# Kernel tuning notes

Hardware: AMD Instinct MI355X
Metric: run time of the kernel (lower is better)

The kernel has to match this reference:

```python
import jax, jax.numpy as jnp
import numpy as np

N = 200000      # number of source simplices (columns of B)
M_SEG = 100000  # number of target simplices (rows of B)
NNZ = 400000    # ~2 nonzeros per column for a boundary operator
C_IN = 256
C_OUT = 256


def setup_inputs() -> dict:
    key = jax.random.key(0)
    k1, k2, k3, k4, k5 = jax.random.split(key, 5)
    x_src = jax.random.normal(k1, (N, C_IN), dtype=jnp.float32)
    W = jax.random.normal(k2, (C_IN, C_OUT), dtype=jnp.float32) / np.sqrt(C_IN)
    b_vals = jax.random.normal(k3, (NNZ,), dtype=jnp.float32)
    b_rows = jax.random.randint(k4, (NNZ,), 0, M_SEG, dtype=jnp.int32)
    b_cols = jax.random.randint(k5, (NNZ,), 0, N, dtype=jnp.int32)
    return {"x_src": x_src, "W": W, "b_vals": b_vals,
            "b_rows": b_rows, "b_cols": b_cols, "M": M_SEG}


def reference(x_src, W, b_vals, b_rows, b_cols, M):
    # Dense projection: nn.Linear(in, out, bias=False) -> x @ W
    x_proj = x_src @ W                                  # [N, C_out]
    # Sparse boundary matmul: out[r] += v * x_proj[c] for each (r, c, v) in B
    msgs = b_vals[:, None] * x_proj[b_cols]             # [nnz, C_out] gather
    out = jax.ops.segment_sum(msgs, b_rows, num_segments=M)  # [M, C_out] scatter-add
    return out
```

## Files before the change

### kernel.cpp

```cpp
#include <hip/hip_runtime.h>


typedef short bf16x8 __attribute__((ext_vector_type(8)));
typedef float f32x4  __attribute__((ext_vector_type(4)));

#define BM 64

static __device__ __forceinline__ unsigned short f2bf(float f) {
    union { float f; unsigned u; } a; a.f = f;
    unsigned r = a.u + 0x7FFFu + ((a.u >> 16) & 1u);
    return (unsigned short)(r >> 16);
}

__global__ __launch_bounds__(256) void wtrans_kernel(
    const float* __restrict__ W, unsigned short* __restrict__ Wt)
{
    int k = blockIdx.x;
    int n = threadIdx.x;
    Wt[(size_t)n * 256 + k] = f2bf(W[(size_t)k * 256 + n]);
}

__global__ __launch_bounds__(256) void hist_kernel(
    const int* __restrict__ b_rows, int* __restrict__ cnt, int nnz)
{
    int i = blockIdx.x * 256 + threadIdx.x;
    if (i < nnz) atomicAdd(&cnt[b_rows[i]], 1);
}

__global__ __launch_bounds__(1024) void scan_part_kernel(
    const int* __restrict__ cnt, int* __restrict__ partials, int M)
{
    int tid = threadIdx.x;
    int base = blockIdx.x * 4096;
    int s = 0;
    #pragma unroll
    for (int k = 0; k < 4; ++k) {
        int i = base + k * 1024 + tid;
        if (i < M) s += cnt[i];
    }
    #pragma unroll
    for (int d = 1; d < 64; d <<= 1) s += __shfl_xor(s, d);
    __shared__ int wsum[16];
    int lane = tid & 63, wid = tid >> 6;
    if (lane == 0) wsum[wid] = s;
    __syncthreads();
    if (tid == 0) {
        int t = 0;
        #pragma unroll
        for (int w = 0; w < 16; ++w) t += wsum[w];
        partials[blockIdx.x] = t;
    }
}

__global__ __launch_bounds__(64) void scan_mid_kernel(
    int* __restrict__ partials, int* __restrict__ off, int np, int M)
{
    int lane = threadIdx.x;
    int v = (lane < np) ? partials[lane] : 0;
    int x = v;
    #pragma unroll
    for (int d = 1; d < 64; d <<= 1) { int y = __shfl_up(x, d); if (lane >= d) x += y; }
    if (lane < np) partials[lane] = x - v;
    if (lane == 63) off[M] = x;
}

__global__ __launch_bounds__(1024) void scan_apply_kernel(
    const int* __restrict__ cnt, const int* __restrict__ partials,
    int* __restrict__ off, int* __restrict__ cursor, int M)
{
    int tid = threadIdx.x;
    int base = blockIdx.x * 4096 + tid * 4;
    int4 v = make_int4(0, 0, 0, 0);
    if (base + 3 < M) v = *reinterpret_cast<const int4*>(cnt + base);
    else {
        if (base + 0 < M) v.x = cnt[base + 0];
        if (base + 1 < M) v.y = cnt[base + 1];
        if (base + 2 < M) v.z = cnt[base + 2];
    }
    int s1 = v.x + v.y, s2 = s1 + v.z, tsum = s2 + v.w;
    int x = tsum;
    int lane = tid & 63, wid = tid >> 6;
    #pragma unroll
    for (int d = 1; d < 64; d <<= 1) { int y = __shfl_up(x, d); if (lane >= d) x += y; }
    __shared__ int wsum[16];
    if (lane == 63) wsum[wid] = x;
    __syncthreads();
    if (wid == 0 && lane < 16) {
        int w = wsum[lane];
        int xx = w;
        #pragma unroll
        for (int d = 1; d < 16; d <<= 1) { int y = __shfl_up(xx, d); if (lane >= d) xx += y; }
        wsum[lane] = xx - w;
    }
    __syncthreads();
    int excl = (x - tsum) + wsum[wid] + partials[blockIdx.x];
    int o0 = excl, o1 = excl + v.x, o2 = excl + s1, o3 = excl + s2;
    if (base + 0 < M) { off[base + 0] = o0; cursor[base + 0] = o0; }
    if (base + 1 < M) { off[base + 1] = o1; cursor[base + 1] = o1; }
    if (base + 2 < M) { off[base + 2] = o2; cursor[base + 2] = o2; }
    if (base + 3 < M) { off[base + 3] = o3; cursor[base + 3] = o3; }
}

__global__ __launch_bounds__(256) void fill_kernel(
    const float* __restrict__ b_vals, const int* __restrict__ b_rows,
    const int* __restrict__ b_cols, int* __restrict__ cursor,
    int* __restrict__ csr_col, float* __restrict__ csr_val, int nnz)
{
    int i = blockIdx.x * 256 + threadIdx.x;
    if (i < nnz) {
        int r = b_rows[i];
        int pos = atomicAdd(&cursor[r], 1);
        csr_col[pos] = b_cols[i];
        csr_val[pos] = b_vals[i];
    }
}

__global__ __launch_bounds__(256) void fused_kernel(
    const float* __restrict__ x_src, const float* __restrict__ csr_val,
    const int* __restrict__ csr_col, const int* __restrict__ off,
    const unsigned short* __restrict__ Wt, float* __restrict__ out, int M)
{
    __shared__ __align__(16) unsigned char Alds[BM * 512];

    int lane = threadIdx.x & 63;
    int wid  = threadIdx.x >> 6;
    int r0   = blockIdx.x * BM;

    const float4* x4 = reinterpret_cast<const float4*>(x_src);
    for (int i = 0; i < 16; ++i) {
        int row = wid * 16 + i;
        int r = r0 + row;
        float4 acc = make_float4(0.f, 0.f, 0.f, 0.f);
        if (r < M) {
            int s = off[r], e = off[r + 1];
            for (int j = s; j < e; ++j) {
                int c = csr_col[j];
                float v = csr_val[j];
                float4 xs = x4[(size_t)c * 64 + lane];
                acc.x += v * xs.x; acc.y += v * xs.y;
                acc.z += v * xs.z; acc.w += v * xs.w;
            }
        }
        ushort4 h;
        h.x = f2bf(acc.x); h.y = f2bf(acc.y); h.z = f2bf(acc.z); h.w = f2bf(acc.w);
        int byte = row * 512 + lane * 8;
        byte ^= (row & 7) << 4;
        *reinterpret_cast<ushort4*>(Alds + byte) = h;
    }
    __syncthreads();

    f32x4 acc[4][4] = {};
    const char* wt = reinterpret_cast<const char*>(Wt);
    int nbase = wid * 64;
    int arow15 = lane & 15;
    int kgrp   = (lane >> 4) * 16;

    for (int s = 0; s < 8; ++s) {
        bf16x8 a[4], b[4];
        #pragma unroll
        for (int m = 0; m < 4; ++m) {
            int row = m * 16 + arow15;
            int byte = row * 512 + s * 64 + kgrp;
            byte ^= (row & 7) << 4;
            a[m] = *reinterpret_cast<const bf16x8*>(Alds + byte);
        }
        #pragma unroll
        for (int t = 0; t < 4; ++t) {
            int n = nbase + t * 16 + arow15;
            b[t] = *reinterpret_cast<const bf16x8*>(wt + (size_t)n * 512 + s * 64 + kgrp);
        }
        #pragma unroll
        for (int m = 0; m < 4; ++m)
            #pragma unroll
            for (int t = 0; t < 4; ++t)
                acc[m][t] = __builtin_amdgcn_mfma_f32_16x16x32_bf16(a[m], b[t], acc[m][t], 0, 0, 0);
    }

    #pragma unroll
    for (int m = 0; m < 4; ++m) {
        int rowb = r0 + m * 16 + (lane >> 4) * 4;
        #pragma unroll
        for (int r = 0; r < 4; ++r) {
            if (rowb + r < M) {
                #pragma unroll
                for (int t = 0; t < 4; ++t)
                    out[(size_t)(rowb + r) * 256 + nbase + t * 16 + arow15] = acc[m][t][r];
            }
        }
    }
}

extern "C" void kernel_launch(void* const* d_in, const int* in_sizes, int n_in,
                              void* d_out, int out_size, void* d_ws, size_t ws_size,
                              hipStream_t stream) {
    const float* x_src  = (const float*)d_in[0];
    const float* W      = (const float*)d_in[1];
    const float* b_vals = (const float*)d_in[2];
    const int*   b_rows = (const int*)d_in[3];
    const int*   b_cols = (const int*)d_in[4];

    const int C = 256;
    const int M = out_size / C;
    const int nnz = in_sizes[2];

    char* ws = (char*)d_ws;
    unsigned short* Wt = (unsigned short*)ws;           ws += 256 * 256 * 2;
    int*   cnt     = (int*)ws;                          ws += (size_t)M * 4;
    int*   off     = (int*)ws;                          ws += (size_t)(M + 1) * 4;
    int*   cursor  = (int*)ws;                          ws += (size_t)M * 4;
    int*   partials= (int*)ws;                          ws += 64 * 4;
    int*   csr_col = (int*)ws;                          ws += (size_t)nnz * 4;
    float* csr_val = (float*)ws;                        ws += (size_t)nnz * 4;

    float* out = (float*)d_out;

    hipMemsetAsync(cnt, 0, (size_t)M * 4, stream);

    wtrans_kernel<<<256, 256, 0, stream>>>(W, Wt);

    int nblk_nnz = (nnz + 255) / 256;
    hist_kernel<<<nblk_nnz, 256, 0, stream>>>(b_rows, cnt, nnz);

    int nb = (M + 4095) / 4096;
    scan_part_kernel<<<nb, 1024, 0, stream>>>(cnt, partials, M);
    scan_mid_kernel<<<1, 64, 0, stream>>>(partials, off, nb, M);
    scan_apply_kernel<<<nb, 1024, 0, stream>>>(cnt, partials, off, cursor, M);

    fill_kernel<<<nblk_nnz, 256, 0, stream>>>(b_vals, b_rows, b_cols, cursor,
                                              csr_col, csr_val, nnz);

    int nblk_fused = (M + BM - 1) / BM;
    fused_kernel<<<nblk_fused, 256, 0, stream>>>(x_src, csr_val, csr_col, off,
                                                 Wt, out, M);
}
```

Baseline: 236.4 us.

## Balance sparse gather across waves with LDS atomics and packed row indices

The gather phase no longer assigns 16 fixed rows to each wave. Instead the block's whole nonzero range is split across waves two entries at a time, and each contribution is added into an fp32 LDS accumulator with atomics. The local row index is packed into the upper bits of the column word, and the row tile is halved to 32 to fit the larger LDS footprint. This targets load imbalance and serial per-row latency chains, at the cost of LDS atomic traffic, an extra pass converting to bf16, and a column range limited to 18 bits.

```diff
diff --git a/kernel.cpp b/kernel.cpp
--- a/kernel.cpp
+++ b/kernel.cpp
@@ -4,7 +4,7 @@
 typedef short bf16x8 __attribute__((ext_vector_type(8)));
 typedef float f32x4  __attribute__((ext_vector_type(4)));
 
-#define BM 64
+#define BM 32
 
 static __device__ __forceinline__ unsigned short f2bf(float f) {
     union { float f; unsigned u; } a; a.f = f;
@@ -104,87 +104,110 @@
 __global__ __launch_bounds__(256) void fill_kernel(
     const float* __restrict__ b_vals, const int* __restrict__ b_rows,
     const int* __restrict__ b_cols, int* __restrict__ cursor,
-    int* __restrict__ csr_col, float* __restrict__ csr_val, int nnz)
+    unsigned int* __restrict__ csr_packed, float* __restrict__ csr_val, int nnz)
 {
     int i = blockIdx.x * 256 + threadIdx.x;
     if (i < nnz) {
         int r = b_rows[i];
         int pos = atomicAdd(&cursor[r], 1);
-        csr_col[pos] = b_cols[i];
+        csr_packed[pos] = (unsigned)b_cols[i] | ((unsigned)(r & (BM - 1)) << 18);
         csr_val[pos] = b_vals[i];
     }
 }
 
 __global__ __launch_bounds__(256) void fused_kernel(
     const float* __restrict__ x_src, const float* __restrict__ csr_val,
-    const int* __restrict__ csr_col, const int* __restrict__ off,
+    const unsigned int* __restrict__ csr_packed, const int* __restrict__ off,
     const unsigned short* __restrict__ Wt, float* __restrict__ out, int M)
 {
-    __shared__ __align__(16) unsigned char Alds[BM * 512];
-
-    int lane = threadIdx.x & 63;
-    int wid  = threadIdx.x >> 6;
-    int r0   = blockIdx.x * BM;
-
-    const float4* x4 = reinterpret_cast<const float4*>(x_src);
-    for (int i = 0; i < 16; ++i) {
-        int row = wid * 16 + i;
-        int r = r0 + row;
-        float4 acc = make_float4(0.f, 0.f, 0.f, 0.f);
-        if (r < M) {
-            int s = off[r], e = off[r + 1];
-            for (int j = s; j < e; ++j) {
-                int c = csr_col[j];
-                float v = csr_val[j];
-                float4 xs = x4[(size_t)c * 64 + lane];
-                acc.x += v * xs.x; acc.y += v * xs.y;
-                acc.z += v * xs.z; acc.w += v * xs.w;
-            }
-        }
-        ushort4 h;
-        h.x = f2bf(acc.x); h.y = f2bf(acc.y); h.z = f2bf(acc.z); h.w = f2bf(acc.w);
-        int byte = row * 512 + lane * 8;
-        byte ^= (row & 7) << 4;
-        *reinterpret_cast<ushort4*>(Alds + byte) = h;
-    }
-    __syncthreads();
-
-    f32x4 acc[4][4] = {};
+    __shared__ __align__(16) float accf[BM * 256];
+    __shared__ __align__(16) unsigned char Ab[BM * 512];
+
+    int tid = threadIdx.x;
+    int lane = tid & 63, wid = tid >> 6;
+    int r0 = blockIdx.x * BM;
+
+    f32x4* az = reinterpret_cast<f32x4*>(accf);
+    #pragma unroll
+    for (int i = 0; i < (BM * 256 / 4) / 256; ++i)
+        az[i * 256 + tid] = (f32x4){0.f, 0.f, 0.f, 0.f};
+    __syncthreads();
+
+    int s_blk = off[r0];
+    int e_blk = off[min(r0 + BM, M)];
+
+    for (int j0 = s_blk + wid * 2; j0 < e_blk; j0 += 8) {
+        int j1 = j0 + 1;
+        bool has1 = (j1 < e_blk);
+        unsigned p0 = csr_packed[j0];
+        float    v0 = csr_val[j0];
+        unsigned p1 = has1 ? csr_packed[j1] : p0;
+        float    v1 = has1 ? csr_val[j1] : 0.f;
+        int c0 = (int)(p0 & 0x3FFFFu), a0 = (int)(p0 >> 18);
+        int c1 = (int)(p1 & 0x3FFFFu), a1 = (int)(p1 >> 18);
+
+        const float* s0 = x_src + (size_t)c0 * 256 + lane;
+        const float* s1 = x_src + (size_t)c1 * 256 + lane;
+        float g00 = s0[0], g01 = s0[64], g02 = s0[128], g03 = s0[192];
+        float g10 = s1[0], g11 = s1[64], g12 = s1[128], g13 = s1[192];
+
+        float* d0 = accf + a0 * 256 + lane;
+        float* d1 = accf + a1 * 256 + lane;
+        atomicAdd(d0 +   0, v0 * g00);
+        atomicAdd(d0 +  64, v0 * g01);
+        atomicAdd(d0 + 128, v0 * g02);
+        atomicAdd(d0 + 192, v0 * g03);
+        atomicAdd(d1 +   0, v1 * g10);
+        atomicAdd(d1 +  64, v1 * g11);
+        atomicAdd(d1 + 128, v1 * g12);
+        atomicAdd(d1 + 192, v1 * g13);
+    }
+    __syncthreads();
+
+    for (int e = tid * 2; e < BM * 256; e += 512) {
+        int row = e >> 8, ch = e & 255;
+        float2 f = *reinterpret_cast<const float2*>(accf + row * 256 + ch);
+        unsigned u = (unsigned)f2bf(f.x) | ((unsigned)f2bf(f.y) << 16);
+        int byte = row * 512 + ((ch * 2) ^ ((row & 7) << 4));
+        *reinterpret_cast<unsigned*>(Ab + byte) = u;
+    }
+    __syncthreads();
+
+    f32x4 acc[2][4] = {};
     const char* wt = reinterpret_cast<const char*>(Wt);
     int nbase = wid * 64;
-    int arow15 = lane & 15;
-    int kgrp   = (lane >> 4) * 16;
+    int arow = lane & 15;
+    int kgrp = (lane >> 4) * 16;
 
     for (int s = 0; s < 8; ++s) {
-        bf16x8 a[4], b[4];
-        #pragma unroll
-        for (int m = 0; m < 4; ++m) {
-            int row = m * 16 + arow15;
-            int byte = row * 512 + s * 64 + kgrp;
-            byte ^= (row & 7) << 4;
-            a[m] = *reinterpret_cast<const bf16x8*>(Alds + byte);
+        bf16x8 a[2], b[4];
+        #pragma unroll
+        for (int m = 0; m < 2; ++m) {
+            int row = m * 16 + arow;
+            int byte = row * 512 + ((s * 64 + kgrp) ^ ((row & 7) << 4));
+            a[m] = *reinterpret_cast<const bf16x8*>(Ab + byte);
         }
         #pragma unroll
         for (int t = 0; t < 4; ++t) {
-            int n = nbase + t * 16 + arow15;
+            int n = nbase + t * 16 + arow;
             b[t] = *reinterpret_cast<const bf16x8*>(wt + (size_t)n * 512 + s * 64 + kgrp);
         }
         #pragma unroll
-        for (int m = 0; m < 4; ++m)
+        for (int m = 0; m < 2; ++m)
             #pragma unroll
             for (int t = 0; t < 4; ++t)
                 acc[m][t] = __builtin_amdgcn_mfma_f32_16x16x32_bf16(a[m], b[t], acc[m][t], 0, 0, 0);
     }
 
     #pragma unroll
-    for (int m = 0; m < 4; ++m) {
+    for (int m = 0; m < 2; ++m) {
         int rowb = r0 + m * 16 + (lane >> 4) * 4;
         #pragma unroll
         for (int r = 0; r < 4; ++r) {
             if (rowb + r < M) {
                 #pragma unroll
                 for (int t = 0; t < 4; ++t)
-                    out[(size_t)(rowb + r) * 256 + nbase + t * 16 + arow15] = acc[m][t][r];
+                    out[(size_t)(rowb + r) * 256 + nbase + t * 16 + arow] = acc[m][t][r];
             }
         }
     }
@@ -209,7 +232,7 @@
     int*   off     = (int*)ws;                          ws += (size_t)(M + 1) * 4;
     int*   cursor  = (int*)ws;                          ws += (size_t)M * 4;
     int*   partials= (int*)ws;                          ws += 64 * 4;
-    int*   csr_col = (int*)ws;                          ws += (size_t)nnz * 4;
+    unsigned int* csr_packed = (unsigned int*)ws;       ws += (size_t)nnz * 4;
     float* csr_val = (float*)ws;                        ws += (size_t)nnz * 4;
 
     float* out = (float*)d_out;
@@ -227,9 +250,9 @@
     scan_apply_kernel<<<nb, 1024, 0, stream>>>(cnt, partials, off, cursor, M);
 
     fill_kernel<<<nblk_nnz, 256, 0, stream>>>(b_vals, b_rows, b_cols, cursor,
-                                              csr_col, csr_val, nnz);
+                                              csr_packed, csr_val, nnz);
 
     int nblk_fused = (M + BM - 1) / BM;
-    fused_kernel<<<nblk_fused, 256, 0, stream>>>(x_src, csr_val, csr_col, off,
+    fused_kernel<<<nblk_fused, 256, 0, stream>>>(x_src, csr_val, csr_packed, off,
                                                  Wt, out, M);
 }
```

New measurement: 627.0 us. 165% more time.

## Split fused gather+GEMM into separate gather and GEMM kernels with chunking

Applied to the files above, without the earlier changes.

The fused kernel, where each block gathered 64 rows serially per wave into LDS before the MFMA GEMM, is split into two kernels. A gather kernel with one wave per row and 8-way unrolled independent loads writes bf16 rows to a workspace buffer, and a GEMM kernel reads them back from global memory. Rows are processed in chunks sized to the available workspace. This raises gather parallelism and memory-level parallelism but adds a global round trip for the intermediate and extra launches.

```diff
diff --git a/kernel.cpp b/kernel.cpp
--- a/kernel.cpp
+++ b/kernel.cpp
@@ -3,8 +3,6 @@
 
 typedef short bf16x8 __attribute__((ext_vector_type(8)));
 typedef float f32x4  __attribute__((ext_vector_type(4)));
-
-#define BM 64
 
 static __device__ __forceinline__ unsigned short f2bf(float f) {
     union { float f; unsigned u; } a; a.f = f;
@@ -115,59 +113,70 @@
     }
 }
 
-__global__ __launch_bounds__(256) void fused_kernel(
+__global__ __launch_bounds__(256) void gather_kernel(
     const float* __restrict__ x_src, const float* __restrict__ csr_val,
     const int* __restrict__ csr_col, const int* __restrict__ off,
-    const unsigned short* __restrict__ Wt, float* __restrict__ out, int M)
-{
-    __shared__ __align__(16) unsigned char Alds[BM * 512];
-
+    unsigned short* __restrict__ tmp, int r_base, int nrows)
+{
+    int wrow = blockIdx.x * 4 + (threadIdx.x >> 6);
+    if (wrow >= nrows) return;
     int lane = threadIdx.x & 63;
-    int wid  = threadIdx.x >> 6;
-    int r0   = blockIdx.x * BM;
-
+    int row = r_base + wrow;
+
+    int s = off[row], e = off[row + 1];
     const float4* x4 = reinterpret_cast<const float4*>(x_src);
-    for (int i = 0; i < 16; ++i) {
-        int row = wid * 16 + i;
-        int r = r0 + row;
-        float4 acc = make_float4(0.f, 0.f, 0.f, 0.f);
-        if (r < M) {
-            int s = off[r], e = off[r + 1];
-            for (int j = s; j < e; ++j) {
-                int c = csr_col[j];
-                float v = csr_val[j];
-                float4 xs = x4[(size_t)c * 64 + lane];
-                acc.x += v * xs.x; acc.y += v * xs.y;
-                acc.z += v * xs.z; acc.w += v * xs.w;
-            }
-        }
-        ushort4 h;
-        h.x = f2bf(acc.x); h.y = f2bf(acc.y); h.z = f2bf(acc.z); h.w = f2bf(acc.w);
-        int byte = row * 512 + lane * 8;
-        byte ^= (row & 7) << 4;
-        *reinterpret_cast<ushort4*>(Alds + byte) = h;
-    }
-    __syncthreads();
+    float4 acc = make_float4(0.f, 0.f, 0.f, 0.f);
+
+    for (int j = s; j < e; j += 8) {
+        int   c[8]; float v[8];
+        #pragma unroll
+        for (int t = 0; t < 8; ++t) {
+            int jj = j + t;
+            int jc = (jj < e) ? jj : s;
+            c[t] = csr_col[jc];
+            v[t] = (jj < e) ? csr_val[jc] : 0.f;
+        }
+        float4 xs[8];
+        #pragma unroll
+        for (int t = 0; t < 8; ++t)
+            xs[t] = x4[(size_t)c[t] * 64 + lane];
+        #pragma unroll
+        for (int t = 0; t < 8; ++t) {
+            acc.x += v[t] * xs[t].x; acc.y += v[t] * xs[t].y;
+            acc.z += v[t] * xs[t].z; acc.w += v[t] * xs[t].w;
+        }
+    }
+
+    ushort4 h;
+    h.x = f2bf(acc.x); h.y = f2bf(acc.y); h.z = f2bf(acc.z); h.w = f2bf(acc.w);
+    *reinterpret_cast<ushort4*>(tmp + (size_t)wrow * 256 + lane * 4) = h;
+}
+
+__global__ __launch_bounds__(256) void gemm_kernel(
+    const unsigned short* __restrict__ tmp, const unsigned short* __restrict__ Wt,
+    float* __restrict__ out, int r_base, int nrows)
+{
+    int lane = threadIdx.x & 63, wid = threadIdx.x >> 6;
+    int m0 = blockIdx.x * 64;
+    int nbase = wid * 64;
+    int arow = lane & 15;
+    int kbyte = (lane >> 4) * 16;
+
+    const char* at = reinterpret_cast<const char*>(tmp);
+    const char* wt = reinterpret_cast<const char*>(Wt);
 
     f32x4 acc[4][4] = {};
-    const char* wt = reinterpret_cast<const char*>(Wt);
-    int nbase = wid * 64;
-    int arow15 = lane & 15;
-    int kgrp   = (lane >> 4) * 16;
-
     for (int s = 0; s < 8; ++s) {
         bf16x8 a[4], b[4];
         #pragma unroll
         for (int m = 0; m < 4; ++m) {
-            int row = m * 16 + arow15;
-            int byte = row * 512 + s * 64 + kgrp;
-            byte ^= (row & 7) << 4;
-            a[m] = *reinterpret_cast<const bf16x8*>(Alds + byte);
+            int row = m0 + m * 16 + arow;
+            a[m] = *reinterpret_cast<const bf16x8*>(at + (size_t)row * 512 + s * 64 + kbyte);
         }
         #pragma unroll
         for (int t = 0; t < 4; ++t) {
-            int n = nbase + t * 16 + arow15;
-            b[t] = *reinterpret_cast<const bf16x8*>(wt + (size_t)n * 512 + s * 64 + kgrp);
+            int n = nbase + t * 16 + arow;
+            b[t] = *reinterpret_cast<const bf16x8*>(wt + (size_t)n * 512 + s * 64 + kbyte);
         }
         #pragma unroll
         for (int m = 0; m < 4; ++m)
@@ -178,13 +187,13 @@
 
     #pragma unroll
     for (int m = 0; m < 4; ++m) {
-        int rowb = r0 + m * 16 + (lane >> 4) * 4;
+        int rl = m0 + m * 16 + (lane >> 4) * 4;
         #pragma unroll
         for (int r = 0; r < 4; ++r) {
-            if (rowb + r < M) {
+            if (rl + r < nrows) {
                 #pragma unroll
                 for (int t = 0; t < 4; ++t)
-                    out[(size_t)(rowb + r) * 256 + nbase + t * 16 + arow15] = acc[m][t][r];
+                    out[(size_t)(r_base + rl + r) * 256 + nbase + t * 16 + arow] = acc[m][t][r];
             }
         }
     }
@@ -211,6 +220,16 @@
     int*   partials= (int*)ws;                          ws += 64 * 4;
     int*   csr_col = (int*)ws;                          ws += (size_t)nnz * 4;
     float* csr_val = (float*)ws;                        ws += (size_t)nnz * 4;
+    ws = (char*)(((size_t)ws + 63) & ~(size_t)63);
+    unsigned short* tmp = (unsigned short*)ws;
+
+    size_t used = (size_t)(ws - (char*)d_ws);
+    size_t avail = (ws_size > used) ? (ws_size - used) : 0;
+    long long cr = (long long)(avail / 512) - 64;
+    if (cr < 64) cr = 64;
+    if (cr > M) cr = M;
+    int chunk_rows = (int)(cr & ~63LL);
+    if (chunk_rows < 64) chunk_rows = 64;
 
     float* out = (float*)d_out;
 
@@ -229,7 +248,10 @@
     fill_kernel<<<nblk_nnz, 256, 0, stream>>>(b_vals, b_rows, b_cols, cursor,
                                               csr_col, csr_val, nnz);
 
-    int nblk_fused = (M + BM - 1) / BM;
-    fused_kernel<<<nblk_fused, 256, 0, stream>>>(x_src, csr_val, csr_col, off,
-                                                 Wt, out, M);
-}
+    for (int r0 = 0; r0 < M; r0 += chunk_rows) {
+        int nr = (M - r0 < chunk_rows) ? (M - r0) : chunk_rows;
+        gather_kernel<<<(nr + 3) / 4, 256, 0, stream>>>(
+            x_src, csr_val, csr_col, off, tmp, r0, nr);
+        gemm_kernel<<<(nr + 63) / 64, 256, 0, stream>>>(tmp, Wt, out, r0, nr);
+    }
+}
```

After: 209.4 us. -11.4%, faster.

## Project all source rows to bf16 first, then gather-sum projected rows

Applied to the files above, without the earlier changes.

The single fused kernel, which gathered fp32 source rows, summed them per target row and then ran an MFMA projection, is replaced by two kernels. A dense MFMA projection of all N source rows writes a bf16 intermediate, and a separate per-row gather kernel accumulates the weighted bf16 projected rows into the fp32 output, batching 8 neighbours at a time. The aim is to turn the random fp32 gather (1 KB per nonzero) into a streaming read of x plus a random gather of half-size bf16 rows that may sit in the large last-level cache. In exchange it does twice the GEMM rows, adds a 100 MB intermediate write and read, and rounds each projected row to bf16 before summation.

```diff
diff --git a/kernel.cpp b/kernel.cpp
--- a/kernel.cpp
+++ b/kernel.cpp
@@ -3,13 +3,16 @@
 
 typedef short bf16x8 __attribute__((ext_vector_type(8)));
 typedef float f32x4  __attribute__((ext_vector_type(4)));
-
-#define BM 64
 
 static __device__ __forceinline__ unsigned short f2bf(float f) {
     union { float f; unsigned u; } a; a.f = f;
     unsigned r = a.u + 0x7FFFu + ((a.u >> 16) & 1u);
     return (unsigned short)(r >> 16);
+}
+
+static __device__ __forceinline__ float bf2f(unsigned short h) {
+    union { unsigned u; float f; } a; a.u = (unsigned)h << 16;
+    return a.f;
 }
 
 __global__ __launch_bounds__(256) void wtrans_kernel(
@@ -115,58 +118,43 @@
     }
 }
 
-__global__ __launch_bounds__(256) void fused_kernel(
-    const float* __restrict__ x_src, const float* __restrict__ csr_val,
-    const int* __restrict__ csr_col, const int* __restrict__ off,
-    const unsigned short* __restrict__ Wt, float* __restrict__ out, int M)
-{
-    __shared__ __align__(16) unsigned char Alds[BM * 512];
-
-    int lane = threadIdx.x & 63;
-    int wid  = threadIdx.x >> 6;
-    int r0   = blockIdx.x * BM;
-
-    const float4* x4 = reinterpret_cast<const float4*>(x_src);
+__global__ __launch_bounds__(256) void proj_kernel(
+    const float* __restrict__ X, const unsigned short* __restrict__ Wt,
+    unsigned short* __restrict__ xp)
+{
+    __shared__ __align__(16) unsigned char Ab[64 * 512];
+    int tid = threadIdx.x, lane = tid & 63, wid = tid >> 6;
+    int r0 = blockIdx.x * 64;
+
+    #pragma unroll
     for (int i = 0; i < 16; ++i) {
         int row = wid * 16 + i;
-        int r = r0 + row;
-        float4 acc = make_float4(0.f, 0.f, 0.f, 0.f);
-        if (r < M) {
-            int s = off[r], e = off[r + 1];
-            for (int j = s; j < e; ++j) {
-                int c = csr_col[j];
-                float v = csr_val[j];
-                float4 xs = x4[(size_t)c * 64 + lane];
-                acc.x += v * xs.x; acc.y += v * xs.y;
-                acc.z += v * xs.z; acc.w += v * xs.w;
-            }
-        }
+        float4 f = *reinterpret_cast<const float4*>(
+            X + (size_t)(r0 + row) * 256 + lane * 4);
         ushort4 h;
-        h.x = f2bf(acc.x); h.y = f2bf(acc.y); h.z = f2bf(acc.z); h.w = f2bf(acc.w);
-        int byte = row * 512 + lane * 8;
-        byte ^= (row & 7) << 4;
-        *reinterpret_cast<ushort4*>(Alds + byte) = h;
+        h.x = f2bf(f.x); h.y = f2bf(f.y); h.z = f2bf(f.z); h.w = f2bf(f.w);
+        int byte = row * 512 + ((lane * 8) ^ ((row & 7) << 4));
+        *reinterpret_cast<ushort4*>(Ab + byte) = h;
     }
     __syncthreads();
 
     f32x4 acc[4][4] = {};
     const char* wt = reinterpret_cast<const char*>(Wt);
     int nbase = wid * 64;
-    int arow15 = lane & 15;
-    int kgrp   = (lane >> 4) * 16;
+    int arow = lane & 15;
+    int kgrp = (lane >> 4) * 16;
 
     for (int s = 0; s < 8; ++s) {
         bf16x8 a[4], b[4];
         #pragma unroll
         for (int m = 0; m < 4; ++m) {
-            int row = m * 16 + arow15;
-            int byte = row * 512 + s * 64 + kgrp;
-            byte ^= (row & 7) << 4;
-            a[m] = *reinterpret_cast<const bf16x8*>(Alds + byte);
+            int row = m * 16 + arow;
+            int byte = row * 512 + ((s * 64 + kgrp) ^ ((row & 7) << 4));
+            a[m] = *reinterpret_cast<const bf16x8*>(Ab + byte);
         }
         #pragma unroll
         for (int t = 0; t < 4; ++t) {
-            int n = nbase + t * 16 + arow15;
+            int n = nbase + t * 16 + arow;
             b[t] = *reinterpret_cast<const bf16x8*>(wt + (size_t)n * 512 + s * 64 + kgrp);
         }
         #pragma unroll
@@ -176,18 +164,61 @@
                 acc[m][t] = __builtin_amdgcn_mfma_f32_16x16x32_bf16(a[m], b[t], acc[m][t], 0, 0, 0);
     }
 
+    int hi = lane >> 4;
     #pragma unroll
     for (int m = 0; m < 4; ++m) {
-        int rowb = r0 + m * 16 + (lane >> 4) * 4;
-        #pragma unroll
-        for (int r = 0; r < 4; ++r) {
-            if (rowb + r < M) {
-                #pragma unroll
-                for (int t = 0; t < 4; ++t)
-                    out[(size_t)(rowb + r) * 256 + nbase + t * 16 + arow15] = acc[m][t][r];
+        #pragma unroll
+        for (int rr = 0; rr < 4; ++rr) {
+            int row = r0 + m * 16 + hi * 4 + rr;
+            ushort4 h;
+            h.x = f2bf(acc[m][0][rr]);
+            h.y = f2bf(acc[m][1][rr]);
+            h.z = f2bf(acc[m][2][rr]);
+            h.w = f2bf(acc[m][3][rr]);
+            *reinterpret_cast<ushort4*>(xp + (size_t)row * 256 + wid * 64 + arow * 4) = h;
+        }
+    }
+}
+
+__global__ __launch_bounds__(256) void gather_kernel(
+    const unsigned short* __restrict__ xp, const float* __restrict__ csr_val,
+    const int* __restrict__ csr_col, const int* __restrict__ off,
+    float* __restrict__ out, int M)
+{
+    int row = blockIdx.x * 4 + (threadIdx.x >> 6);
+    if (row >= M) return;
+    int lane = threadIdx.x & 63;
+
+    int s = off[row], e = off[row + 1];
+    float a0 = 0.f, a1 = 0.f, a2 = 0.f, a3 = 0.f;
+
+    for (int j = s; j < e; j += 8) {
+        int nb = e - j;
+        int c[8]; float v[8]; ushort4 xs[8];
+        #pragma unroll
+        for (int t = 0; t < 8; ++t)
+            if (t < nb) { c[t] = csr_col[j + t]; v[t] = csr_val[j + t]; }
+        #pragma unroll
+        for (int t = 0; t < 8; ++t)
+            if (t < nb)
+                xs[t] = *reinterpret_cast<const ushort4*>(
+                    xp + (size_t)c[t] * 256 + lane * 4);
+        #pragma unroll
+        for (int t = 0; t < 8; ++t)
+            if (t < nb) {
+                a0 += v[t] * bf2f(xs[t].x);
+                a1 += v[t] * bf2f(xs[t].y);
+                a2 += v[t] * bf2f(xs[t].z);
+                a3 += v[t] * bf2f(xs[t].w);
             }
-        }
-    }
+    }
+
+    int col0 = (lane >> 4) * 64 + (lane & 15);
+    float* o = out + (size_t)row * 256;
+    o[col0 +  0] = a0;
+    o[col0 + 16] = a1;
+    o[col0 + 32] = a2;
+    o[col0 + 48] = a3;
 }
 
 extern "C" void kernel_launch(void* const* d_in, const int* in_sizes, int n_in,
@@ -202,6 +233,7 @@
     const int C = 256;
     const int M = out_size / C;
     const int nnz = in_sizes[2];
+    const int N = in_sizes[0] / C;
 
     char* ws = (char*)d_ws;
     unsigned short* Wt = (unsigned short*)ws;           ws += 256 * 256 * 2;
@@ -211,6 +243,8 @@
     int*   partials= (int*)ws;                          ws += 64 * 4;
     int*   csr_col = (int*)ws;                          ws += (size_t)nnz * 4;
     float* csr_val = (float*)ws;                        ws += (size_t)nnz * 4;
+    ws = (char*)(((size_t)ws + 63) & ~(size_t)63);
+    unsigned short* xp = (unsigned short*)ws;
 
     float* out = (float*)d_out;
 
@@ -229,7 +263,7 @@
     fill_kernel<<<nblk_nnz, 256, 0, stream>>>(b_vals, b_rows, b_cols, cursor,
                                               csr_col, csr_val, nnz);
 
-    int nblk_fused = (M + BM - 1) / BM;
-    fused_kernel<<<nblk_fused, 256, 0, stream>>>(x_src, csr_val, csr_col, off,
-                                                 Wt, out, M);
-}
+    proj_kernel<<<(N + 63) / 64, 256, 0, stream>>>(x_src, Wt, xp);
+
+    gather_kernel<<<(M + 3) / 4, 256, 0, stream>>>(xp, csr_val, csr_col, off, out, M);
+}
```

Measured after the change: 220.3 us. 6.8% less time.
